# Kernel tuning notes

Hardware: AMD Instinct MI355X
Metric: run time of the kernel (lower is better)

Reference implementation:

```python
import jax, jax.numpy as jnp
import numpy as np

N = 50000      # nodes
E = 800000     # edges
IN = 256       # in_dim
HID = 64       # num_hidden
H0 = 4         # heads[0]
H1 = 1         # heads[1]
OUT1 = HID * H0  # 256, last GATConv out_feats
C = 64         # num_classes
NEG_SLOPE = 0.2


def setup_inputs() -> dict:
    ks = jax.random.split(jax.random.key(0), 13)
    s = 0.05
    return {
        "x":   jax.random.normal(ks[0], (N, IN), jnp.float32),
        "src": jax.random.randint(ks[1], (E,), 0, N, jnp.int32),
        "dst": jax.random.randint(ks[2], (E,), 0, N, jnp.int32),
        # layer 0: GATConv(IN, HID, H0)
        "W0":  jax.random.normal(ks[3], (IN, H0 * HID), jnp.float32) * s,
        "al0": jax.random.normal(ks[4], (H0, HID), jnp.float32) * s,
        "ar0": jax.random.normal(ks[5], (H0, HID), jnp.float32) * s,
        "b0":  jnp.zeros((H0 * HID,), jnp.float32),
        # layer 1: GATConv(H0*HID, OUT1, H1), residual (identity since in == H1*OUT1)
        "W1":  jax.random.normal(ks[6], (H0 * HID, H1 * OUT1), jnp.float32) * s,
        "al1": jax.random.normal(ks[7], (H1, OUT1), jnp.float32) * s,
        "ar1": jax.random.normal(ks[8], (H1, OUT1), jnp.float32) * s,
        "b1":  jnp.zeros((H1 * OUT1,), jnp.float32),
        # final classifier Linear(OUT1, C)
        "Wl":  jax.random.normal(ks[9], (OUT1, C), jnp.float32) * s,
        "bl":  jnp.zeros((C,), jnp.float32),
    }


def gat_conv(h, src, dst, W, al, ar, b, heads, out, residual, act):
    # ft: projected per-head features [N, H, D]
    ft = (h @ W).reshape(-1, heads, out)
    el = jnp.sum(ft * al, axis=-1)          # [N, H]
    er = jnp.sum(ft * ar, axis=-1)          # [N, H]
    e = jax.nn.leaky_relu(el[src] + er[dst], NEG_SLOPE)  # [E, H]
    # edge softmax grouped by destination node
    emax = jax.ops.segment_max(e, dst, num_segments=N)
    a = jnp.exp(e - emax[dst])
    asum = jax.ops.segment_sum(a, dst, num_segments=N)
    alpha = a / asum[dst]                   # [E, H]
    msg = alpha[:, :, None] * ft[src]       # [E, H, D]
    rst = jax.ops.segment_sum(msg, dst, num_segments=N)  # [N, H, D]
    if residual:  # identity residual (in_feats == heads*out)
        rst = rst + h.reshape(-1, heads, out)
    rst = rst + b.reshape(1, heads, out)
    if act is not None:
        rst = act(rst)
    return rst


def reference(x, src, dst, W0, al0, ar0, b0, W1, al1, ar1, b1, Wl, bl):
    h = gat_conv(x, src, dst, W0, al0, ar0, b0, H0, HID, False, jax.nn.elu)
    h = h.reshape(N, -1)                    # flatten(1) -> [N, H0*HID]
    h = gat_conv(h, src, dst, W1, al1, ar1, b1, H1, OUT1, True, None)
    h = h.mean(axis=1)                      # mean over heads -> [N, OUT1]
    logits = h @ Wl + bl
    return (logits, h)
```

## Files before the change

kernel.cpp:

```cpp
#include <hip/hip_runtime.h>
#include <hip/hip_bf16.h>
#include <stdint.h>

#define NNODES 50000
#define NEDGES 800000
#define CH     256
#define NCLS   64
#define DCAP   64
#define RB     224

typedef __attribute__((ext_vector_type(8))) short  short8;
typedef __attribute__((ext_vector_type(4))) float  floatx4;

__device__ __forceinline__ float bf2f(unsigned short u) {
    union { unsigned int i; float f; } v; v.i = ((unsigned int)u) << 16; return v.f;
}
__device__ __forceinline__ unsigned short f2bf(float f) {
    union { float f; unsigned int i; } v; v.f = f;
    unsigned int x = v.i;
    return (unsigned short)((x + 0x7fffu + ((x >> 16) & 1u)) >> 16);
}

__device__ __forceinline__ void gl_lds16(const void* g, void* l) {
    __builtin_amdgcn_global_load_lds(
        (const __attribute__((address_space(1))) unsigned int*)g,
        (__attribute__((address_space(3))) unsigned int*)l, 16, 0, 0);
}

__global__ void k_setup(const float* __restrict__ W0, const float* __restrict__ W1,
                        const float* __restrict__ Wl, const float* __restrict__ x,
                        unsigned short* __restrict__ w0t, unsigned short* __restrict__ w1t,
                        unsigned short* __restrict__ wlt, unsigned short* __restrict__ xbf,
                        int* __restrict__ cnt) {
    int i = blockIdx.x * 256 + threadIdx.x;
    if (i < 65536) {
        int r = i >> 8, c = i & 255;
        w0t[c * 256 + r] = f2bf(W0[i]);
    } else if (i < 131072) {
        int j = i - 65536;
        int r = j >> 8, c = j & 255;
        w1t[c * 256 + r] = f2bf(W1[j]);
    } else if (i < 147456) {
        int j = i - 131072;
        int r = j >> 6, c = j & 63;
        wlt[c * 256 + r] = f2bf(Wl[j]);
    } else if (i < 147456 + NNODES) {
        cnt[i - 147456] = 0;
    } else {
        int j = i - (147456 + NNODES);
        if (j < NNODES * CH / 8) {
            const float4* xp = (const float4*)(x + (size_t)j * 8);
            float4 v0 = xp[0], v1 = xp[1];
            ushort4 o0, o1;
            o0.x = f2bf(v0.x); o0.y = f2bf(v0.y); o0.z = f2bf(v0.z); o0.w = f2bf(v0.w);
            o1.x = f2bf(v1.x); o1.y = f2bf(v1.y); o1.z = f2bf(v1.z); o1.w = f2bf(v1.w);
            *(ushort4*)(xbf + (size_t)j * 8)     = o0;
            *(ushort4*)(xbf + (size_t)j * 8 + 4) = o1;
        }
    }
}

__global__ void k_scatter(const int* __restrict__ dst, const int* __restrict__ src,
                          int* __restrict__ cnt, int* __restrict__ esrc) {
    int e = blockIdx.x * 256 + threadIdx.x;
    if (e < NEDGES) {
        int d = dst[e];
        if ((unsigned)d < NNODES) {
            int p = atomicAdd(&cnt[d], 1);
            if (p < DCAP) esrc[(size_t)d * DCAP + p] = src[e];
        }
    }
}

template<int BN, bool AF32, bool OUTF32, int HEL>
__global__ __launch_bounds__(512, 1) void k_gemmw(
        const void* __restrict__ Av, const unsigned short* __restrict__ BT,
        const float* __restrict__ bias,
        float* __restrict__ Cf, unsigned short* __restrict__ Cb,
        int M, int N,
        const float* __restrict__ al, const float* __restrict__ ar,
        float* __restrict__ el, float* __restrict__ er) {
    constexpr int NT     = BN / 16;
    constexpr int ROUNDS = (BN * 512) / 8192;
    __shared__ unsigned short Bw[BN * 256];
    const int t  = threadIdx.x;
    const int w  = t >> 6, l = t & 63;
    const int lm = l & 15, lg = l >> 4;

#pragma unroll
    for (int r = 0; r < ROUNDS; ++r) {
        int g   = r * 8192 + t * 16;
        int row = g >> 9;
        int bir = g & 511;
        int sb  = (g & ~511) | (bir ^ ((row & 7) << 4));
        gl_lds16((const char*)BT + sb, (char*)Bw + r * 8192 + w * 1024);
    }

    const int m0    = blockIdx.x * RB;
    const int Mb    = (m0 + RB < M) ? (m0 + RB) : M;
    const int tile0 = m0 + w * 32;
    const bool active = (w < 7) && (tile0 < Mb);

    const unsigned short* Ab = (const unsigned short*)Av;
    const float*          Af = (const float*)Av;
    short8 af[2][8];
#pragma unroll
    for (int g = 0; g < 2; ++g) {
        int arow = tile0 + g * 16 + lm;
        bool ok = active && (arow < M);
#pragma unroll
        for (int ks = 0; ks < 8; ++ks) {
            if (AF32) {
                short8 v = (short8)0;
                if (ok) {
                    const float* ap = Af + (size_t)arow * 256 + ks * 32 + lg * 8;
                    float4 v0 = *(const float4*)(ap), v1 = *(const float4*)(ap + 4);
                    v[0] = (short)f2bf(v0.x); v[1] = (short)f2bf(v0.y);
                    v[2] = (short)f2bf(v0.z); v[3] = (short)f2bf(v0.w);
                    v[4] = (short)f2bf(v1.x); v[5] = (short)f2bf(v1.y);
                    v[6] = (short)f2bf(v1.z); v[7] = (short)f2bf(v1.w);
                }
                af[g][ks] = v;
            } else {
                af[g][ks] = ok ? *(const short8*)(Ab + (size_t)arow * 256 + ks * 32 + lg * 8)
                               : (short8)0;
            }
        }
    }

    __syncthreads();
    if (!active) return;

    floatx4 acc[2][NT];
#pragma unroll
    for (int g = 0; g < 2; ++g)
#pragma unroll
        for (int nt = 0; nt < NT; ++nt) acc[g][nt] = (floatx4)0.0f;

    const int kx   = (lm >> 2) & 1;
    const int coff = (lg * 16) ^ ((lm & 3) << 4);
    const char* Bb = (const char*)Bw;
#pragma unroll
    for (int ks = 0; ks < 8; ++ks) {
        int kk = (ks ^ kx) * 64;
#pragma unroll
        for (int nt = 0; nt < NT; ++nt) {
            short8 bf = *(const short8*)(Bb + (nt * 16 + lm) * 512 + kk + coff);
            acc[0][nt] = __builtin_amdgcn_mfma_f32_16x16x32_bf16(af[0][ks], bf, acc[0][nt], 0, 0, 0);
            acc[1][nt] = __builtin_amdgcn_mfma_f32_16x16x32_bf16(af[1][ks], bf, acc[1][nt], 0, 0, 0);
        }
    }

    float alv[HEL > 0 ? NT : 1], arv[HEL > 0 ? NT : 1];
    if (HEL > 0) {
#pragma unroll
        for (int nt = 0; nt < NT; ++nt) {
            alv[nt] = al[nt * 16 + lm];
            arv[nt] = ar[nt * 16 + lm];
        }
    }
#pragma unroll
    for (int g = 0; g < 2; ++g)
#pragma unroll
        for (int j = 0; j < 4; ++j) {
            int row = tile0 + g * 16 + lg * 4 + j;
            if (row < Mb) {
#pragma unroll
                for (int nt = 0; nt < NT; ++nt) {
                    int gcol = nt * 16 + lm;
                    float v = acc[g][nt][j];
                    if (bias) v += bias[gcol];
                    if (OUTF32) Cf[(size_t)row * N + gcol] = v;
                    else        Cb[(size_t)row * N + gcol] = f2bf(v);
                }
                if (HEL > 0) {
#pragma unroll
                    for (int h = 0; h < HEL; ++h) {
                        float sl = 0.f, sr = 0.f;
#pragma unroll
                        for (int q = 0; q < NT / HEL; ++q) {
                            int nt = h * (NT / HEL) + q;
                            float v = acc[g][nt][j];
                            sl += v * alv[nt];
                            sr += v * arv[nt];
                        }
#pragma unroll
                        for (int mm = 1; mm < 16; mm <<= 1) {
                            sl += __shfl_xor(sl, mm, 64);
                            sr += __shfl_xor(sr, mm, 64);
                        }
                        if (lm == 0) {
                            el[(size_t)row * HEL + h] = sl;
                            er[(size_t)row * HEL + h] = sr;
                        }
                    }
                }
            }
        }
}

template<int H, bool ELU, bool RESID>
__global__ __launch_bounds__(256) void k_agg5(
        const unsigned short* __restrict__ ft,
        const float* __restrict__ el, const float* __restrict__ er,
        const int* __restrict__ cnt,
        const int* __restrict__ esrc,
        const unsigned short* __restrict__ resid16,
        const float* __restrict__ bias,
        unsigned short* __restrict__ out_bf,
        float* __restrict__ out_f) {
    int w = threadIdx.x >> 6;
    int n = blockIdx.x * 4 + w;
    int l = threadIdx.x & 63;
    int c = 4 * l;
    int st = n * DCAP;
    int dg = __builtin_amdgcn_readfirstlane(cnt[n]);
    if (dg > DCAP) dg = DCAP;
    if (dg < 0) dg = 0;
    float a0 = 0.f, a1 = 0.f, a2 = 0.f, a3 = 0.f, wsum = 0.f;
    const unsigned short* ftc = ft + c;

    if (H == 1) {
        float ern = er[n];
        for (int i = 0; i < dg; i += 64) {
            int idx = i + l;
            int sv = 0; float wv = 0.f;
            if (idx < dg) {
                sv = esrc[st + idx];
                float xv = el[sv] + ern;
                xv = (xv > 0.f) ? xv : 0.2f * xv;
                xv = fminf(xv, 60.f);
                wv = __expf(xv);
            }
            wsum += wv;
            int jmax = dg - i; if (jmax > 64) jmax = 64;
            int j = 0;
            for (; j + 4 <= jmax; j += 4) {
                int s0 = __builtin_amdgcn_readlane(sv, j + 0);
                int s1 = __builtin_amdgcn_readlane(sv, j + 1);
                int s2 = __builtin_amdgcn_readlane(sv, j + 2);
                int s3 = __builtin_amdgcn_readlane(sv, j + 3);
                float w0 = __int_as_float(__builtin_amdgcn_readlane(__float_as_int(wv), j + 0));
                float w1 = __int_as_float(__builtin_amdgcn_readlane(__float_as_int(wv), j + 1));
                float w2 = __int_as_float(__builtin_amdgcn_readlane(__float_as_int(wv), j + 2));
                float w3 = __int_as_float(__builtin_amdgcn_readlane(__float_as_int(wv), j + 3));
                ushort4 f0 = *(const ushort4*)(ftc + (size_t)s0 * CH);
                ushort4 f1 = *(const ushort4*)(ftc + (size_t)s1 * CH);
                ushort4 f2 = *(const ushort4*)(ftc + (size_t)s2 * CH);
                ushort4 f3 = *(const ushort4*)(ftc + (size_t)s3 * CH);
                a0 += w0 * bf2f(f0.x) + w1 * bf2f(f1.x) + w2 * bf2f(f2.x) + w3 * bf2f(f3.x);
                a1 += w0 * bf2f(f0.y) + w1 * bf2f(f1.y) + w2 * bf2f(f2.y) + w3 * bf2f(f3.y);
                a2 += w0 * bf2f(f0.z) + w1 * bf2f(f1.z) + w2 * bf2f(f2.z) + w3 * bf2f(f3.z);
                a3 += w0 * bf2f(f0.w) + w1 * bf2f(f1.w) + w2 * bf2f(f2.w) + w3 * bf2f(f3.w);
            }
            for (; j < jmax; ++j) {
                int s0 = __builtin_amdgcn_readlane(sv, j);
                float w0 = __int_as_float(__builtin_amdgcn_readlane(__float_as_int(wv), j));
                ushort4 f0 = *(const ushort4*)(ftc + (size_t)s0 * CH);
                a0 += w0 * bf2f(f0.x); a1 += w0 * bf2f(f0.y);
                a2 += w0 * bf2f(f0.z); a3 += w0 * bf2f(f0.w);
            }
        }
#pragma unroll
        for (int m = 1; m < 64; m <<= 1) wsum += __shfl_xor(wsum, m, 64);
    } else {
        int head = l & 3, slot = l >> 2;
        int h = l >> 4;
        float ern = er[n * 4 + head];
        for (int i = 0; i < dg; i += 16) {
            int idx = i + slot;
            int sv = 0; float wv = 0.f;
            if (idx < dg) {
                sv = esrc[st + idx];
                float xv = el[sv * 4 + head] + ern;
                xv = (xv > 0.f) ? xv : 0.2f * xv;
                xv = fminf(xv, 60.f);
                wv = __expf(xv);
            }
            wsum += wv;
            int jmax = dg - i; if (jmax > 16) jmax = 16;
            int j = 0;
            for (; j + 4 <= jmax; j += 4) {
                int s0 = __builtin_amdgcn_readlane(sv, 4 * (j + 0));
                int s1 = __builtin_amdgcn_readlane(sv, 4 * (j + 1));
                int s2 = __builtin_amdgcn_readlane(sv, 4 * (j + 2));
                int s3 = __builtin_amdgcn_readlane(sv, 4 * (j + 3));
                float w0 = __shfl(wv, 4 * (j + 0) + h, 64);
                float w1 = __shfl(wv, 4 * (j + 1) + h, 64);
                float w2 = __shfl(wv, 4 * (j + 2) + h, 64);
                float w3 = __shfl(wv, 4 * (j + 3) + h, 64);
                ushort4 f0 = *(const ushort4*)(ftc + (size_t)s0 * CH);
                ushort4 f1 = *(const ushort4*)(ftc + (size_t)s1 * CH);
                ushort4 f2 = *(const ushort4*)(ftc + (size_t)s2 * CH);
                ushort4 f3 = *(const ushort4*)(ftc + (size_t)s3 * CH);
                a0 += w0 * bf2f(f0.x) + w1 * bf2f(f1.x) + w2 * bf2f(f2.x) + w3 * bf2f(f3.x);
                a1 += w0 * bf2f(f0.y) + w1 * bf2f(f1.y) + w2 * bf2f(f2.y) + w3 * bf2f(f3.y);
                a2 += w0 * bf2f(f0.z) + w1 * bf2f(f1.z) + w2 * bf2f(f2.z) + w3 * bf2f(f3.z);
                a3 += w0 * bf2f(f0.w) + w1 * bf2f(f1.w) + w2 * bf2f(f2.w) + w3 * bf2f(f3.w);
            }
            for (; j < jmax; ++j) {
                int s0 = __builtin_amdgcn_readlane(sv, 4 * j);
                float w0 = __shfl(wv, 4 * j + h, 64);
                ushort4 f0 = *(const ushort4*)(ftc + (size_t)s0 * CH);
                a0 += w0 * bf2f(f0.x); a1 += w0 * bf2f(f0.y);
                a2 += w0 * bf2f(f0.z); a3 += w0 * bf2f(f0.w);
            }
        }
#pragma unroll
        for (int m = 4; m < 64; m <<= 1) wsum += __shfl_xor(wsum, m, 64);
        wsum = __shfl(wsum, l >> 4, 64);
    }
    float inv = (wsum > 1e-30f) ? 1.0f / wsum : 0.0f;
    a0 *= inv; a1 *= inv; a2 *= inv; a3 *= inv;
    if (RESID) {
        ushort4 r = *(const ushort4*)(resid16 + (size_t)n * CH + c);
        a0 += bf2f(r.x); a1 += bf2f(r.y); a2 += bf2f(r.z); a3 += bf2f(r.w);
    }
    {
        float4 b = *(const float4*)(bias + c);
        a0 += b.x; a1 += b.y; a2 += b.z; a3 += b.w;
    }
    if (ELU) {
        a0 = (a0 > 0.f) ? a0 : __expf(a0) - 1.f;
        a1 = (a1 > 0.f) ? a1 : __expf(a1) - 1.f;
        a2 = (a2 > 0.f) ? a2 : __expf(a2) - 1.f;
        a3 = (a3 > 0.f) ? a3 : __expf(a3) - 1.f;
    }
    if (out_bf) {
        ushort4 ov; ov.x = f2bf(a0); ov.y = f2bf(a1); ov.z = f2bf(a2); ov.w = f2bf(a3);
        *(ushort4*)(out_bf + (size_t)n * CH + c) = ov;
    }
    if (out_f) {
        *(float4*)(out_f + (size_t)n * CH + c) = make_float4(a0, a1, a2, a3);
    }
}


extern "C" void kernel_launch(void* const* d_in, const int* in_sizes, int n_in,
                              void* d_out, int out_size, void* d_ws, size_t ws_size,
                              hipStream_t stream) {
    const float* x   = (const float*)d_in[0];
    const int*   src = (const int*)d_in[1];
    const int*   dst = (const int*)d_in[2];
    const float* W0  = (const float*)d_in[3];
    const float* al0 = (const float*)d_in[4];
    const float* ar0 = (const float*)d_in[5];
    const float* b0  = (const float*)d_in[6];
    const float* W1  = (const float*)d_in[7];
    const float* al1 = (const float*)d_in[8];
    const float* ar1 = (const float*)d_in[9];
    const float* b1  = (const float*)d_in[10];
    const float* Wl  = (const float*)d_in[11];
    const float* bl  = (const float*)d_in[12];

    float* out_logits = (float*)d_out;
    float* out_h      = out_logits + (size_t)NNODES * NCLS;

    unsigned short* xbf = (unsigned short*)out_h;

    char* ws = (char*)d_ws;
    size_t o = 0;
    auto alloc = [&](size_t b) { char* p = ws + o; o += (b + 255) & ~(size_t)255; return p; };
    unsigned short* ft   = (unsigned short*)alloc((size_t)NNODES * CH * 2);
    unsigned short* h0bf = (unsigned short*)alloc((size_t)NNODES * CH * 2);
    int*            esrc = (int*)alloc((size_t)NNODES * DCAP * 4);
    unsigned short* w0t  = (unsigned short*)alloc(256 * 256 * 2);
    unsigned short* w1t  = (unsigned short*)alloc(256 * 256 * 2);
    unsigned short* wlt  = (unsigned short*)alloc(64 * 256 * 2);
    int*            cnt  = (int*)alloc((size_t)NNODES * 4);
    float*          el0  = (float*)alloc((size_t)NNODES * 4 * 4);
    float*          er0  = (float*)alloc((size_t)NNODES * 4 * 4);
    float*          el1  = (float*)alloc((size_t)NNODES * 4);
    float*          er1  = (float*)alloc((size_t)NNODES * 4);

    int setup_items = 147456 + NNODES + NNODES * CH / 8;
    k_setup<<<(setup_items + 255) / 256, 256, 0, stream>>>(W0, W1, Wl, x,
                                                           w0t, w1t, wlt, xbf, cnt);
    k_scatter<<<(NEDGES + 255) / 256, 256, 0, stream>>>(dst, src, cnt, esrc);

    int gm = (NNODES + RB - 1) / RB;
    k_gemmw<256, false, false, 4><<<gm, 512, 0, stream>>>(
        xbf, w0t, nullptr, nullptr, ft, NNODES, CH, al0, ar0, el0, er0);
    k_agg5<4, true, false><<<NNODES / 4, 256, 0, stream>>>(
        ft, el0, er0, cnt, esrc, nullptr, b0, h0bf, nullptr);
    k_gemmw<256, false, false, 1><<<gm, 512, 0, stream>>>(
        h0bf, w1t, nullptr, nullptr, ft, NNODES, CH, al1, ar1, el1, er1);
    k_agg5<1, false, true><<<NNODES / 4, 256, 0, stream>>>(
        ft, el1, er1, cnt, esrc, h0bf, b1, nullptr, out_h);
    k_gemmw<64, true, true, 0><<<gm, 512, 0, stream>>>(
        out_h, wlt, bl, out_logits, nullptr, NNODES, NCLS,
        nullptr, nullptr, nullptr, nullptr);
}
```

Measured before the change: 345.0 us.

## Split GEMM columns across a 2D grid and halve aggregation launches

The projection GEMMs now tile over output columns via blockIdx.y, with 128-column tiles and 2 blocks per CU in the launch bounds. This doubles the number of blocks and shrinks the LDS footprint per block, aiming for better occupancy. For the single-head layer, the attention logit partial sums from each column tile are combined with atomicAdd, so el1 and er1 are now zeroed in the setup kernel. The final classifier GEMM uses one 16-row group per wave, and each aggregation pass is split into two launches over node halves, which adds launch overhead and atomic traffic.

Measured after the change: 367.6 us. 6.6% more time.

```diff
diff --git a/kernel.cpp b/kernel.cpp
--- a/kernel.cpp
+++ b/kernel.cpp
@@ -7,7 +7,6 @@
 #define CH     256
 #define NCLS   64
 #define DCAP   64
-#define RB     224
 
 typedef __attribute__((ext_vector_type(8))) short  short8;
 typedef __attribute__((ext_vector_type(4))) float  floatx4;
@@ -31,7 +30,8 @@
                         const float* __restrict__ Wl, const float* __restrict__ x,
                         unsigned short* __restrict__ w0t, unsigned short* __restrict__ w1t,
                         unsigned short* __restrict__ wlt, unsigned short* __restrict__ xbf,
-                        int* __restrict__ cnt) {
+                        int* __restrict__ cnt, float* __restrict__ el1,
+                        float* __restrict__ er1) {
     int i = blockIdx.x * 256 + threadIdx.x;
     if (i < 65536) {
         int r = i >> 8, c = i & 255;
@@ -46,17 +46,19 @@
         wlt[c * 256 + r] = f2bf(Wl[j]);
     } else if (i < 147456 + NNODES) {
         cnt[i - 147456] = 0;
+    } else if (i < 147456 + NNODES + NNODES * CH / 8) {
+        int j = i - (147456 + NNODES);
+        const float4* xp = (const float4*)(x + (size_t)j * 8);
+        float4 v0 = xp[0], v1 = xp[1];
+        ushort4 o0, o1;
+        o0.x = f2bf(v0.x); o0.y = f2bf(v0.y); o0.z = f2bf(v0.z); o0.w = f2bf(v0.w);
+        o1.x = f2bf(v1.x); o1.y = f2bf(v1.y); o1.z = f2bf(v1.z); o1.w = f2bf(v1.w);
+        *(ushort4*)(xbf + (size_t)j * 8)     = o0;
+        *(ushort4*)(xbf + (size_t)j * 8 + 4) = o1;
     } else {
-        int j = i - (147456 + NNODES);
-        if (j < NNODES * CH / 8) {
-            const float4* xp = (const float4*)(x + (size_t)j * 8);
-            float4 v0 = xp[0], v1 = xp[1];
-            ushort4 o0, o1;
-            o0.x = f2bf(v0.x); o0.y = f2bf(v0.y); o0.z = f2bf(v0.z); o0.w = f2bf(v0.w);
-            o1.x = f2bf(v1.x); o1.y = f2bf(v1.y); o1.z = f2bf(v1.z); o1.w = f2bf(v1.w);
-            *(ushort4*)(xbf + (size_t)j * 8)     = o0;
-            *(ushort4*)(xbf + (size_t)j * 8 + 4) = o1;
-        }
+        int j2 = i - (147456 + NNODES + NNODES * CH / 8);
+        if (j2 < NNODES) el1[j2] = 0.f;
+        else if (j2 < 2 * NNODES) er1[j2 - NNODES] = 0.f;
     }
 }
 
@@ -72,8 +74,8 @@
     }
 }
 
-template<int BN, bool AF32, bool OUTF32, int HEL>
-__global__ __launch_bounds__(512, 1) void k_gemmw(
+template<int BN, int G2, bool AF32, bool OUTF32, int HEL>
+__global__ __launch_bounds__(512, 2) void k_gemmw2(
         const void* __restrict__ Av, const unsigned short* __restrict__ BT,
         const float* __restrict__ bias,
         float* __restrict__ Cf, unsigned short* __restrict__ Cb,
@@ -81,32 +83,34 @@
         const float* __restrict__ al, const float* __restrict__ ar,
         float* __restrict__ el, float* __restrict__ er) {
     constexpr int NT     = BN / 16;
-    constexpr int ROUNDS = (BN * 512) / 8192;
+    constexpr int RBT    = 7 * 16 * G2;
+    constexpr int ROUNDS = BN / 16;
     __shared__ unsigned short Bw[BN * 256];
     const int t  = threadIdx.x;
     const int w  = t >> 6, l = t & 63;
     const int lm = l & 15, lg = l >> 4;
-
+    const int n0 = blockIdx.y * BN;
+
+    const char* Bsrc = (const char*)BT + (size_t)n0 * 512;
 #pragma unroll
     for (int r = 0; r < ROUNDS; ++r) {
-        int g   = r * 8192 + t * 16;
-        int row = g >> 9;
-        int bir = g & 511;
-        int sb  = (g & ~511) | (bir ^ ((row & 7) << 4));
-        gl_lds16((const char*)BT + sb, (char*)Bw + r * 8192 + w * 1024);
-    }
-
-    const int m0    = blockIdx.x * RB;
-    const int Mb    = (m0 + RB < M) ? (m0 + RB) : M;
-    const int tile0 = m0 + w * 32;
-    const bool active = (w < 7) && (tile0 < Mb);
+        int g    = r * 8192 + t * 16;
+        int lrow = g >> 9;
+        int bir  = g & 511;
+        int sb   = (g & ~511) | (bir ^ ((lrow & 7) << 4));
+        gl_lds16(Bsrc + sb, (char*)Bw + r * 8192 + w * 1024);
+    }
+
+    const int m0    = blockIdx.x * RBT;
+    const int tile0 = m0 + w * 16 * G2;
+    const bool active = (w < 7) && (tile0 < M);
 
     const unsigned short* Ab = (const unsigned short*)Av;
     const float*          Af = (const float*)Av;
-    short8 af[2][8];
-#pragma unroll
-    for (int g = 0; g < 2; ++g) {
-        int arow = tile0 + g * 16 + lm;
+    short8 af[G2][8];
+#pragma unroll
+    for (int g2 = 0; g2 < G2; ++g2) {
+        int arow = tile0 + g2 * 16 + lm;
         bool ok = active && (arow < M);
 #pragma unroll
         for (int ks = 0; ks < 8; ++ks) {
@@ -120,10 +124,10 @@
                     v[4] = (short)f2bf(v1.x); v[5] = (short)f2bf(v1.y);
                     v[6] = (short)f2bf(v1.z); v[7] = (short)f2bf(v1.w);
                 }
-                af[g][ks] = v;
+                af[g2][ks] = v;
             } else {
-                af[g][ks] = ok ? *(const short8*)(Ab + (size_t)arow * 256 + ks * 32 + lg * 8)
-                               : (short8)0;
+                af[g2][ks] = ok ? *(const short8*)(Ab + (size_t)arow * 256 + ks * 32 + lg * 8)
+                                : (short8)0;
             }
         }
     }
@@ -131,11 +135,11 @@
     __syncthreads();
     if (!active) return;
 
-    floatx4 acc[2][NT];
-#pragma unroll
-    for (int g = 0; g < 2; ++g)
-#pragma unroll
-        for (int nt = 0; nt < NT; ++nt) acc[g][nt] = (floatx4)0.0f;
+    floatx4 acc[G2][NT];
+#pragma unroll
+    for (int g2 = 0; g2 < G2; ++g2)
+#pragma unroll
+        for (int nt = 0; nt < NT; ++nt) acc[g2][nt] = (floatx4)0.0f;
 
     const int kx   = (lm >> 2) & 1;
     const int coff = (lg * 16) ^ ((lm & 3) << 4);
@@ -146,41 +150,66 @@
 #pragma unroll
         for (int nt = 0; nt < NT; ++nt) {
             short8 bf = *(const short8*)(Bb + (nt * 16 + lm) * 512 + kk + coff);
-            acc[0][nt] = __builtin_amdgcn_mfma_f32_16x16x32_bf16(af[0][ks], bf, acc[0][nt], 0, 0, 0);
-            acc[1][nt] = __builtin_amdgcn_mfma_f32_16x16x32_bf16(af[1][ks], bf, acc[1][nt], 0, 0, 0);
+#pragma unroll
+            for (int g2 = 0; g2 < G2; ++g2)
+                acc[g2][nt] = __builtin_amdgcn_mfma_f32_16x16x32_bf16(af[g2][ks], bf,
+                                                                      acc[g2][nt], 0, 0, 0);
         }
     }
 
     float alv[HEL > 0 ? NT : 1], arv[HEL > 0 ? NT : 1];
-    if (HEL > 0) {
+    if constexpr (HEL > 0) {
 #pragma unroll
         for (int nt = 0; nt < NT; ++nt) {
-            alv[nt] = al[nt * 16 + lm];
-            arv[nt] = ar[nt * 16 + lm];
-        }
-    }
-#pragma unroll
-    for (int g = 0; g < 2; ++g)
+            alv[nt] = al[n0 + nt * 16 + lm];
+            arv[nt] = ar[n0 + nt * 16 + lm];
+        }
+    }
+#pragma unroll
+    for (int g2 = 0; g2 < G2; ++g2)
 #pragma unroll
         for (int j = 0; j < 4; ++j) {
-            int row = tile0 + g * 16 + lg * 4 + j;
-            if (row < Mb) {
+            int row = tile0 + g2 * 16 + lg * 4 + j;
+            if (row < M) {
 #pragma unroll
                 for (int nt = 0; nt < NT; ++nt) {
-                    int gcol = nt * 16 + lm;
-                    float v = acc[g][nt][j];
+                    int gcol = n0 + nt * 16 + lm;
+                    float v = acc[g2][nt][j];
                     if (bias) v += bias[gcol];
                     if (OUTF32) Cf[(size_t)row * N + gcol] = v;
                     else        Cb[(size_t)row * N + gcol] = f2bf(v);
                 }
-                if (HEL > 0) {
-#pragma unroll
-                    for (int h = 0; h < HEL; ++h) {
+                if constexpr (HEL > 0) {
+                    constexpr int D = CH / (HEL > 0 ? HEL : 1);
+                    if constexpr (BN >= D) {
+                        constexpr int HLOC = BN / D;
+                        constexpr int NPH  = NT / HLOC;
+                        int h0 = n0 / D;
+#pragma unroll
+                        for (int hl = 0; hl < HLOC; ++hl) {
+                            float sl = 0.f, sr = 0.f;
+#pragma unroll
+                            for (int q = 0; q < NPH; ++q) {
+                                int nt = hl * NPH + q;
+                                float v = acc[g2][nt][j];
+                                sl += v * alv[nt];
+                                sr += v * arv[nt];
+                            }
+#pragma unroll
+                            for (int mm = 1; mm < 16; mm <<= 1) {
+                                sl += __shfl_xor(sl, mm, 64);
+                                sr += __shfl_xor(sr, mm, 64);
+                            }
+                            if (lm == 0) {
+                                el[(size_t)row * HEL + h0 + hl] = sl;
+                                er[(size_t)row * HEL + h0 + hl] = sr;
+                            }
+                        }
+                    } else {
                         float sl = 0.f, sr = 0.f;
 #pragma unroll
-                        for (int q = 0; q < NT / HEL; ++q) {
-                            int nt = h * (NT / HEL) + q;
-                            float v = acc[g][nt][j];
+                        for (int nt = 0; nt < NT; ++nt) {
+                            float v = acc[g2][nt][j];
                             sl += v * alv[nt];
                             sr += v * arv[nt];
                         }
@@ -190,8 +219,8 @@
                             sr += __shfl_xor(sr, mm, 64);
                         }
                         if (lm == 0) {
-                            el[(size_t)row * HEL + h] = sl;
-                            er[(size_t)row * HEL + h] = sr;
+                            atomicAdd(&el[row], sl);
+                            atomicAdd(&er[row], sr);
                         }
                     }
                 }
@@ -208,9 +237,9 @@
         const unsigned short* __restrict__ resid16,
         const float* __restrict__ bias,
         unsigned short* __restrict__ out_bf,
-        float* __restrict__ out_f) {
+        float* __restrict__ out_f, int nbase) {
     int w = threadIdx.x >> 6;
-    int n = blockIdx.x * 4 + w;
+    int n = nbase + blockIdx.x * 4 + w;
     int l = threadIdx.x & 63;
     int c = 4 * l;
     int st = n * DCAP;
@@ -373,21 +402,28 @@
     float*          el1  = (float*)alloc((size_t)NNODES * 4);
     float*          er1  = (float*)alloc((size_t)NNODES * 4);
 
-    int setup_items = 147456 + NNODES + NNODES * CH / 8;
+    int setup_items = 147456 + NNODES + NNODES * CH / 8 + 2 * NNODES;
     k_setup<<<(setup_items + 255) / 256, 256, 0, stream>>>(W0, W1, Wl, x,
-                                                           w0t, w1t, wlt, xbf, cnt);
+                                                           w0t, w1t, wlt, xbf, cnt, el1, er1);
     k_scatter<<<(NEDGES + 255) / 256, 256, 0, stream>>>(dst, src, cnt, esrc);
 
-    int gm = (NNODES + RB - 1) / RB;
-    k_gemmw<256, false, false, 4><<<gm, 512, 0, stream>>>(
+    int gm2 = (NNODES + 223) / 224;
+    int gm1 = (NNODES + 111) / 112;
+    int ga  = (NNODES / 2) / 4;
+
+    k_gemmw2<128, 2, false, false, 4><<<dim3(gm2, 2), 512, 0, stream>>>(
         xbf, w0t, nullptr, nullptr, ft, NNODES, CH, al0, ar0, el0, er0);
-    k_agg5<4, true, false><<<NNODES / 4, 256, 0, stream>>>(
-        ft, el0, er0, cnt, esrc, nullptr, b0, h0bf, nullptr);
-    k_gemmw<256, false, false, 1><<<gm, 512, 0, stream>>>(
+    k_agg5<4, true, false><<<ga, 256, 0, stream>>>(
+        ft, el0, er0, cnt, esrc, nullptr, b0, h0bf, nullptr, 0);
+    k_agg5<4, true, false><<<ga, 256, 0, stream>>>(
+        ft, el0, er0, cnt, esrc, nullptr, b0, h0bf, nullptr, NNODES / 2);
+    k_gemmw2<128, 2, false, false, 1><<<dim3(gm2, 2), 512, 0, stream>>>(
         h0bf, w1t, nullptr, nullptr, ft, NNODES, CH, al1, ar1, el1, er1);
-    k_agg5<1, false, true><<<NNODES / 4, 256, 0, stream>>>(
-        ft, el1, er1, cnt, esrc, h0bf, b1, nullptr, out_h);
-    k_gemmw<64, true, true, 0><<<gm, 512, 0, stream>>>(
+    k_agg5<1, false, true><<<ga, 256, 0, stream>>>(
+        ft, el1, er1, cnt, esrc, h0bf, b1, nullptr, out_h, 0);
+    k_agg5<1, false, true><<<ga, 256, 0, stream>>>(
+        ft, el1, er1, cnt, esrc, h0bf, b1, nullptr, out_h, NNODES / 2);
+    k_gemmw2<64, 1, true, true, 0><<<dim3(gm1, 1), 512, 0, stream>>>(
         out_h, wlt, bl, out_logits, nullptr, NNODES, NCLS,
         nullptr, nullptr, nullptr, nullptr);
 }
```

## Fuse edge scatter into idle wave of first projection GEMM

Applied to the files above, without the earlier changes.

Removes the standalone scatter kernel that buckets edges by destination. That work now runs on the eighth wave of each layer-0 GEMM block, which has no rows to compute because 7 waves cover the 224-row tile. Each block handles a fixed slice of edges, so the atomics and esrc writes overlap with the MFMA work and one launch is dropped. The cost is extra memory traffic and atomics competing with the GEMM inside the same blocks. Edge order within each bucket stays nondeterministic, as it was before.

Measured after the change: 335.0 us. -2.9%, faster.

```diff
diff --git a/kernel.cpp b/kernel.cpp
--- a/kernel.cpp
+++ b/kernel.cpp
@@ -8,6 +8,7 @@
 #define NCLS   64
 #define DCAP   64
 #define RB     224
+#define EPB    3572
 
 typedef __attribute__((ext_vector_type(8))) short  short8;
 typedef __attribute__((ext_vector_type(4))) float  floatx4;
@@ -60,26 +61,16 @@
     }
 }
 
-__global__ void k_scatter(const int* __restrict__ dst, const int* __restrict__ src,
-                          int* __restrict__ cnt, int* __restrict__ esrc) {
-    int e = blockIdx.x * 256 + threadIdx.x;
-    if (e < NEDGES) {
-        int d = dst[e];
-        if ((unsigned)d < NNODES) {
-            int p = atomicAdd(&cnt[d], 1);
-            if (p < DCAP) esrc[(size_t)d * DCAP + p] = src[e];
-        }
-    }
-}
-
-template<int BN, bool AF32, bool OUTF32, int HEL>
+template<int BN, bool AF32, bool OUTF32, int HEL, bool SCAT>
 __global__ __launch_bounds__(512, 1) void k_gemmw(
         const void* __restrict__ Av, const unsigned short* __restrict__ BT,
         const float* __restrict__ bias,
         float* __restrict__ Cf, unsigned short* __restrict__ Cb,
         int M, int N,
         const float* __restrict__ al, const float* __restrict__ ar,
-        float* __restrict__ el, float* __restrict__ er) {
+        float* __restrict__ el, float* __restrict__ er,
+        const int* __restrict__ edst, const int* __restrict__ esr,
+        int* __restrict__ cnt, int* __restrict__ esrc) {
     constexpr int NT     = BN / 16;
     constexpr int ROUNDS = (BN * 512) / 8192;
     __shared__ unsigned short Bw[BN * 256];
@@ -129,6 +120,36 @@
     }
 
     __syncthreads();
+
+    if (w == 7) {
+        if (SCAT) {
+            int base = blockIdx.x * EPB;
+            int end  = base + EPB; if (end > NEDGES) end = NEDGES;
+            int e = base + l;
+            for (; e + 192 < end; e += 256) {
+                int d0 = edst[e],       s0 = esr[e];
+                int d1 = edst[e + 64],  s1 = esr[e + 64];
+                int d2 = edst[e + 128], s2 = esr[e + 128];
+                int d3 = edst[e + 192], s3 = esr[e + 192];
+                int p0 = ((unsigned)d0 < NNODES) ? atomicAdd(&cnt[d0], 1) : DCAP;
+                int p1 = ((unsigned)d1 < NNODES) ? atomicAdd(&cnt[d1], 1) : DCAP;
+                int p2 = ((unsigned)d2 < NNODES) ? atomicAdd(&cnt[d2], 1) : DCAP;
+                int p3 = ((unsigned)d3 < NNODES) ? atomicAdd(&cnt[d3], 1) : DCAP;
+                if (p0 < DCAP) esrc[(size_t)d0 * DCAP + p0] = s0;
+                if (p1 < DCAP) esrc[(size_t)d1 * DCAP + p1] = s1;
+                if (p2 < DCAP) esrc[(size_t)d2 * DCAP + p2] = s2;
+                if (p3 < DCAP) esrc[(size_t)d3 * DCAP + p3] = s3;
+            }
+            for (; e < end; e += 64) {
+                int d = edst[e];
+                if ((unsigned)d < NNODES) {
+                    int p = atomicAdd(&cnt[d], 1);
+                    if (p < DCAP) esrc[(size_t)d * DCAP + p] = esr[e];
+                }
+            }
+        }
+        return;
+    }
     if (!active) return;
 
     floatx4 acc[2][NT];
@@ -152,7 +173,7 @@
     }
 
     float alv[HEL > 0 ? NT : 1], arv[HEL > 0 ? NT : 1];
-    if (HEL > 0) {
+    if constexpr (HEL > 0) {
 #pragma unroll
         for (int nt = 0; nt < NT; ++nt) {
             alv[nt] = al[nt * 16 + lm];
@@ -173,7 +194,7 @@
                     if (OUTF32) Cf[(size_t)row * N + gcol] = v;
                     else        Cb[(size_t)row * N + gcol] = f2bf(v);
                 }
-                if (HEL > 0) {
+                if constexpr (HEL > 0) {
 #pragma unroll
                     for (int h = 0; h < HEL; ++h) {
                         float sl = 0.f, sr = 0.f;
@@ -376,18 +397,20 @@
     int setup_items = 147456 + NNODES + NNODES * CH / 8;
     k_setup<<<(setup_items + 255) / 256, 256, 0, stream>>>(W0, W1, Wl, x,
                                                            w0t, w1t, wlt, xbf, cnt);
-    k_scatter<<<(NEDGES + 255) / 256, 256, 0, stream>>>(dst, src, cnt, esrc);
 
     int gm = (NNODES + RB - 1) / RB;
-    k_gemmw<256, false, false, 4><<<gm, 512, 0, stream>>>(
-        xbf, w0t, nullptr, nullptr, ft, NNODES, CH, al0, ar0, el0, er0);
+    k_gemmw<256, false, false, 4, true><<<gm, 512, 0, stream>>>(
+        xbf, w0t, nullptr, nullptr, ft, NNODES, CH, al0, ar0, el0, er0,
+        dst, src, cnt, esrc);
     k_agg5<4, true, false><<<NNODES / 4, 256, 0, stream>>>(
         ft, el0, er0, cnt, esrc, nullptr, b0, h0bf, nullptr);
-    k_gemmw<256, false, false, 1><<<gm, 512, 0, stream>>>(
-        h0bf, w1t, nullptr, nullptr, ft, NNODES, CH, al1, ar1, el1, er1);
+    k_gemmw<256, false, false, 1, false><<<gm, 512, 0, stream>>>(
+        h0bf, w1t, nullptr, nullptr, ft, NNODES, CH, al1, ar1, el1, er1,
+        nullptr, nullptr, nullptr, nullptr);
     k_agg5<1, false, true><<<NNODES / 4, 256, 0, stream>>>(
         ft, el1, er1, cnt, esrc, h0bf, b1, nullptr, out_h);
-    k_gemmw<64, true, true, 0><<<gm, 512, 0, stream>>>(
+    k_gemmw<64, true, true, 0, false><<<gm, 512, 0, stream>>>(
         out_h, wlt, bl, out_logits, nullptr, NNODES, NCLS,
+        nullptr, nullptr, nullptr, nullptr,
         nullptr, nullptr, nullptr, nullptr);
 }
```
